# Kernel optimization log

Hardware: AMD Instinct MI355X
Metric: run time of the kernel (lower is better)

Reference implementation:

```python
import jax, jax.numpy as jnp
import numpy as np

E = 8          # num_experts
K = 2          # top_k
CAPF = 1.25    # capacity_factor


def setup_inputs() -> dict:
    key = jax.random.key(0)
    ks = jax.random.split(key, 6)
    B, T, C = 4, 2048, 1024
    x = jax.random.normal(ks[0], (B, T, C), jnp.float32)
    noise = jax.random.normal(ks[1], (B, T, E), jnp.float32)  # stands in for torch.randn_like
    Wr = jax.random.normal(ks[2], (C, E), jnp.float32) * 0.02   # topkroute_linear
    Wn = jax.random.normal(ks[3], (C, E), jnp.float32) * 0.02   # noise_linear
    W1 = jax.random.normal(ks[4], (E, C, 4 * C), jnp.float32) * 0.02  # expert up-proj
    W2 = jax.random.normal(ks[5], (E, 4 * C, C), jnp.float32) * 0.02  # expert down-proj
    return {"x": x, "noise": noise, "Wr": Wr, "Wn": Wn, "W1": W1, "W2": W2}


def reference(x, noise, Wr, Wn, W1, W2):
    B, T, C = x.shape
    N = B * T
    cap = int(N * K / E * CAPF)  # expert_capacity (static)

    # --- NoisyTopkRouter ---
    logits = x @ Wr                                  # [B,T,E]
    noise_logits = x @ Wn                            # [B,T,E]
    noisy = logits + noise * jax.nn.softplus(noise_logits)
    _, idx = jax.lax.top_k(noisy, K)                 # [B,T,K]
    mask_bte = (idx[..., None] == jnp.arange(E)).any(axis=-2)       # [B,T,E]
    gating = jax.nn.softmax(jnp.where(mask_bte, noisy, -jnp.inf), axis=-1)

    flat_x = x.reshape(N, C)
    flat_g = gating.reshape(N, E)

    # --- capacity-limited dispatch (token order, first `cap` per expert) ---
    mask = mask_bte.reshape(N, E).T                  # [E,N]
    rank = jnp.cumsum(mask, axis=1) - 1              # position within expert
    keep = mask & (rank < cap)
    slot = jnp.where(keep, rank, cap)                # overflow -> dump slot `cap`
    tok = jnp.where(keep, jnp.arange(N)[None, :], N) # dropped -> pad token `N`
    s2t = jnp.full((E, cap + 1), N, dtype=jnp.int32)
    s2t = s2t.at[jnp.arange(E)[:, None], slot].set(tok.astype(jnp.int32))[:, :cap]  # [E,cap]

    # --- gather, grouped GEMM (Linear-SiLU-Linear), weight, scatter-add ---
    x_pad = jnp.concatenate([flat_x, jnp.zeros((1, C), flat_x.dtype)], axis=0)
    xin = x_pad[s2t]                                 # [E,cap,C]
    h = jax.nn.silu(jnp.einsum('enc,ech->enh', xin, W1))
    out = jnp.einsum('enh,ehc->enc', h, W2)          # [E,cap,C]
    g_pad = jnp.concatenate([flat_g, jnp.zeros((1, E), flat_g.dtype)], axis=0)
    gate = g_pad[s2t, jnp.arange(E)[:, None]]        # [E,cap]
    weighted = out * gate[..., None]
    upd = jnp.zeros((N + 1, C), x.dtype).at[s2t.reshape(-1)].add(weighted.reshape(-1, C))
    return upd[:N].reshape(B, T, C)
```

## Files before the change

kernel.cpp:

```cpp
#include <hip/hip_runtime.h>
#include <hip/hip_bf16.h>
#include <math.h>

#define C_DIM 1024
#define H_DIM 4096
#define E_NUM 8

typedef __bf16 bf16x8 __attribute__((ext_vector_type(8)));
typedef float f32x4 __attribute__((ext_vector_type(4)));

__device__ __forceinline__ unsigned short f2bf(float f) {
  union { float f; unsigned u; } v; v.f = f;
  unsigned r = v.u + 0x7FFFu + ((v.u >> 16) & 1u);
  return (unsigned short)(r >> 16);
}

__device__ __forceinline__ void gload16(const short* g, short* l) {
  __builtin_amdgcn_global_load_lds(
      (const __attribute__((address_space(1))) unsigned int*)g,
      (__attribute__((address_space(3))) unsigned int*)l, 16, 0, 0);
}

__global__ __launch_bounds__(256) void router_kernel(
    const float* __restrict__ x, const float* __restrict__ noise,
    const float* __restrict__ Wr, const float* __restrict__ Wn,
    int2* __restrict__ idx_out, float2* __restrict__ gate_out, int N)
{
  int t = blockIdx.x;
  int tid = threadIdx.x;
  const float* xrow = x + (size_t)t * C_DIM;
  float accR[E_NUM], accN[E_NUM];
#pragma unroll
  for (int e = 0; e < E_NUM; e++) { accR[e] = 0.f; accN[e] = 0.f; }
  for (int c = tid; c < C_DIM; c += 256) {
    float xv = xrow[c];
    const float* wr = Wr + (size_t)c * E_NUM;
    const float* wn = Wn + (size_t)c * E_NUM;
#pragma unroll
    for (int e = 0; e < E_NUM; e++) {
      accR[e] = fmaf(xv, wr[e], accR[e]);
      accN[e] = fmaf(xv, wn[e], accN[e]);
    }
  }
#pragma unroll
  for (int e = 0; e < E_NUM; e++) {
    for (int off = 32; off > 0; off >>= 1) {
      accR[e] += __shfl_down(accR[e], off, 64);
      accN[e] += __shfl_down(accN[e], off, 64);
    }
  }
  __shared__ float red[4][2 * E_NUM];
  int lane = tid & 63, wave = tid >> 6;
  if (lane == 0) {
#pragma unroll
    for (int e = 0; e < E_NUM; e++) { red[wave][e] = accR[e]; red[wave][E_NUM + e] = accN[e]; }
  }
  __syncthreads();
  if (tid == 0) {
    float ns[E_NUM];
#pragma unroll
    for (int e = 0; e < E_NUM; e++) {
      float lg = red[0][e] + red[1][e] + red[2][e] + red[3][e];
      float nl = red[0][E_NUM + e] + red[1][E_NUM + e] + red[2][E_NUM + e] + red[3][E_NUM + e];
      float sp = fmaxf(nl, 0.f) + log1pf(expf(-fabsf(nl)));
      ns[e] = lg + noise[(size_t)t * E_NUM + e] * sp;
    }
    int i1 = 0; float m1 = ns[0];
    int i2 = -1; float m2 = -INFINITY;
#pragma unroll
    for (int e = 1; e < E_NUM; e++) {
      float v = ns[e];
      if (v > m1) { m2 = m1; i2 = i1; m1 = v; i1 = e; }
      else if (v > m2) { m2 = v; i2 = e; }
    }
    float e2 = expf(m2 - m1);
    float s = 1.f + e2;
    gate_out[t] = make_float2(1.f / s, e2 / s);
    idx_out[t] = make_int2(i1, i2);
  }
}

__global__ __launch_bounds__(256) void scan_kernel(
    const int2* __restrict__ idx, const float2* __restrict__ gates,
    int* __restrict__ s2t, float* __restrict__ gslot, int* __restrict__ counts,
    int N, int cap)
{
  int e = blockIdx.x;
  int tid = threadIdx.x;
  for (int s = tid; s < cap; s += 256) { s2t[(size_t)e * cap + s] = N; gslot[(size_t)e * cap + s] = 0.f; }
  __syncthreads();
  __shared__ int wtot[4];
  int lane = tid & 63, wave = tid >> 6;
  int running = 0;
  for (int base = 0; base < N; base += 256) {
    int t = base + tid;
    int2 ix = idx[t];
    bool flag = (ix.x == e) || (ix.y == e);
    unsigned long long m = __ballot(flag);
    int rank = __popcll(m & ((1ull << lane) - 1ull));
    if (lane == 0) wtot[wave] = __popcll(m);
    __syncthreads();
    int woff = 0;
    for (int w = 0; w < wave; w++) woff += wtot[w];
    int slot = running + woff + rank;
    if (flag && slot < cap) {
      s2t[(size_t)e * cap + slot] = t;
      gslot[(size_t)e * cap + slot] = (ix.x == e) ? gates[t].x : gates[t].y;
    }
    running += wtot[0] + wtot[1] + wtot[2] + wtot[3];
    __syncthreads();
  }
  if (tid == 0) counts[e] = min(running, cap);
}

__global__ __launch_bounds__(256) void convert_x_kernel(
    const float* __restrict__ src, short* __restrict__ dst, int n8)
{
  int i = blockIdx.x * 256 + threadIdx.x;
  if (i >= n8) return;
  const float4* s = (const float4*)src + (size_t)i * 2;
  float4 a = s[0], b = s[1];
  union { unsigned short us[8]; uint4 v; } o;
  o.us[0] = f2bf(a.x); o.us[1] = f2bf(a.y); o.us[2] = f2bf(a.z); o.us[3] = f2bf(a.w);
  o.us[4] = f2bf(b.x); o.us[5] = f2bf(b.y); o.us[6] = f2bf(b.z); o.us[7] = f2bf(b.w);
  ((uint4*)dst)[i] = o.v;
}

__global__ __launch_bounds__(256) void transpose_convert_kernel(
    const float* __restrict__ src, short* __restrict__ dst,
    int R, int Cc)
{
  src += (size_t)blockIdx.z * R * Cc;
  dst += (size_t)blockIdx.z * (size_t)R * Cc;
  __shared__ float tile[64][65];
  int c0 = blockIdx.x * 64, r0 = blockIdx.y * 64;
  int tid = threadIdx.x;
  int tr = tid >> 4, tc = (tid & 15) * 4;
#pragma unroll
  for (int p = 0; p < 4; p++) {
    int r = p * 16 + tr;
    float4 v = *(const float4*)(src + (size_t)(r0 + r) * Cc + c0 + tc);
    tile[r][tc] = v.x; tile[r][tc + 1] = v.y; tile[r][tc + 2] = v.z; tile[r][tc + 3] = v.w;
  }
  __syncthreads();
#pragma unroll
  for (int p = 0; p < 4; p++) {
    int c = p * 16 + tr;
    union { unsigned short us[4]; ushort4 v; } o;
#pragma unroll
    for (int j = 0; j < 4; j++) o.us[j] = f2bf(tile[tc + j][c]);
    *(ushort4*)(dst + (size_t)(c0 + c) * R + r0 + tc) = o.v;
  }
}

template<int MODE>
__global__ __launch_bounds__(512, 2) void gemm_moe(
    const short* __restrict__ Abase, const short* __restrict__ Wt,
    const int* __restrict__ s2t, const float* __restrict__ gslot,
    const int* __restrict__ counts, void* __restrict__ outp,
    int cap, int N, int rows)
{
  __shared__ short As[2][8192];
  __shared__ short Bs[2][8192];

  int flat = blockIdx.x;
  int e = flat & 7;
  int s = flat >> 3;
  int r = s % rows;
  int t = s / rows;
  int c, kc;
  if (MODE == 0) { c = t; kc = 0; }
  else           { c = t & 3; kc = t >> 2; }

  int cnt = counts[e];
  int row0 = r * 256;
  if (row0 >= cnt) return;
  int col0 = c * 256;

  int tid = threadIdx.x;
  int w = tid >> 6, l = tid & 63;
  int wr = w >> 2, wc = w & 3;
  int rowT = tid & 255, kbT = tid >> 8;

  const int NS = 32;

  const short *pA, *pB;
  if (MODE == 0) {
    int tok = min(s2t[(size_t)e * cap + row0 + rowT], N - 1);
    pA = Abase + (size_t)tok * C_DIM;
    pB = Wt + (size_t)e * (C_DIM * H_DIM) + (size_t)(col0 + rowT) * C_DIM;
  } else {
    pA = Abase + ((size_t)e * cap + row0 + rowT) * H_DIM + kc * 1024;
    pB = Wt + (size_t)e * (C_DIM * H_DIM) + (size_t)(col0 + rowT) * H_DIM + kc * 1024;
  }

  int aBase = (l >> 4) * 2048 + (wr * 128 + (l & 15)) * 8;
  int bBase = (l >> 4) * 2048 + (wc * 64 + (l & 15)) * 8;

  f32x4 acc[8][4];
#pragma unroll
  for (int m = 0; m < 8; m++)
#pragma unroll
    for (int n = 0; n < 4; n++) acc[m][n] = 0.f;

#define STAGE(k0, buf) { \
  gload16(pA + (k0) + kbT * 8,       &As[buf][kbT * 2048 + rowT * 8]); \
  gload16(pA + (k0) + (kbT + 2) * 8, &As[buf][(kbT + 2) * 2048 + rowT * 8]); \
  gload16(pB + (k0) + kbT * 8,       &Bs[buf][kbT * 2048 + rowT * 8]); \
  gload16(pB + (k0) + (kbT + 2) * 8, &Bs[buf][(kbT + 2) * 2048 + rowT * 8]); }

  STAGE(0, 0);
  int cur = 0;
#pragma unroll 1
  for (int i = 0; i < NS; ++i) {
    __syncthreads();
    bf16x8 af[8], bg[4];
#pragma unroll
    for (int m = 0; m < 8; m++)
      af[m] = *(const bf16x8*)&As[cur][aBase + m * 128];
#pragma unroll
    for (int n = 0; n < 4; n++)
      bg[n] = *(const bf16x8*)&Bs[cur][bBase + n * 128];
    if (i + 1 < NS) STAGE((i + 1) * 32, cur ^ 1);
#pragma unroll
    for (int m = 0; m < 8; m++)
#pragma unroll
      for (int n = 0; n < 4; n++)
        acc[m][n] = __builtin_amdgcn_mfma_f32_16x16x32_bf16(af[m], bg[n], acc[m][n], 0, 0, 0);
    cur ^= 1;
  }
#undef STAGE

  int orow = row0 + wr * 128 + (l >> 4) * 4;
  int ocol = col0 + wc * 64 + (l & 15);
  if (MODE == 0) {
    short* hE = (short*)outp + (size_t)e * cap * H_DIM;
#pragma unroll
    for (int m = 0; m < 8; m++)
#pragma unroll
      for (int rr = 0; rr < 4; rr++) {
        int slot = orow + m * 16 + rr;
        float g = gslot[(size_t)e * cap + slot];
        size_t rb = (size_t)slot * H_DIM + ocol;
#pragma unroll
        for (int n = 0; n < 4; n++) {
          float v = acc[m][n][rr];
          hE[rb + n * 16] = (short)f2bf(g * (v / (1.f + expf(-v))));
        }
      }
  } else {
    float* out = (float*)outp;
#pragma unroll
    for (int m = 0; m < 8; m++)
#pragma unroll
      for (int rr = 0; rr < 4; rr++) {
        int slot = orow + m * 16 + rr;
        int tok = s2t[(size_t)e * cap + slot];
        if (tok < N) {
          float* op = out + (size_t)tok * C_DIM + ocol;
#pragma unroll
          for (int n = 0; n < 4; n++)
            atomicAdd(op + n * 16, acc[m][n][rr]);
        }
      }
  }
}

extern "C" void kernel_launch(void* const* d_in, const int* in_sizes, int n_in,
                              void* d_out, int out_size, void* d_ws, size_t ws_size,
                              hipStream_t stream)
{
  const float* x     = (const float*)d_in[0];
  const float* noise = (const float*)d_in[1];
  const float* Wr    = (const float*)d_in[2];
  const float* Wn    = (const float*)d_in[3];
  const float* W1    = (const float*)d_in[4];
  const float* W2    = (const float*)d_in[5];
  float* out = (float*)d_out;

  int N = in_sizes[0] / C_DIM;
  int cap = (int)((double)N * 2.0 / E_NUM * 1.25);
  int rows = cap / 256;

  size_t off = 0;
  auto alloc = [&](size_t bytes) -> char* {
    char* r = (char*)d_ws + off;
    off += (bytes + 255) & ~(size_t)255;
    return r;
  };
  int2*   idx    = (int2*)alloc((size_t)N * sizeof(int2));
  float2* gates  = (float2*)alloc((size_t)N * sizeof(float2));
  int*    s2t    = (int*)alloc((size_t)E_NUM * cap * sizeof(int));
  float*  gslot  = (float*)alloc((size_t)E_NUM * cap * sizeof(float));
  int*    counts = (int*)alloc(E_NUM * sizeof(int));
  short*  xbf    = (short*)alloc((size_t)N * C_DIM * sizeof(short));
  short*  W1t    = (short*)alloc((size_t)E_NUM * C_DIM * H_DIM * sizeof(short));
  short*  W2t    = (short*)alloc((size_t)E_NUM * C_DIM * H_DIM * sizeof(short));
  short*  h      = (short*)alloc((size_t)E_NUM * cap * H_DIM * sizeof(short));
  (void)ws_size;

  hipMemsetAsync(d_out, 0, (size_t)out_size * sizeof(float), stream);
  router_kernel<<<N, 256, 0, stream>>>(x, noise, Wr, Wn, idx, gates, N);
  scan_kernel<<<E_NUM, 256, 0, stream>>>(idx, gates, s2t, gslot, counts, N, cap);
  convert_x_kernel<<<(N * C_DIM / 8 + 255) / 256, 256, 0, stream>>>(x, xbf, N * C_DIM / 8);
  transpose_convert_kernel<<<dim3(H_DIM / 64, C_DIM / 64, E_NUM), 256, 0, stream>>>(
      W1, W1t, C_DIM, H_DIM);
  transpose_convert_kernel<<<dim3(C_DIM / 64, H_DIM / 64, E_NUM), 256, 0, stream>>>(
      W2, W2t, H_DIM, C_DIM);

  gemm_moe<0><<<dim3(E_NUM * rows * (H_DIM / 256)), 512, 0, stream>>>(
      xbf, W1t, s2t, gslot, counts, h, cap, N, rows);
  gemm_moe<1><<<dim3(E_NUM * rows * 4 * 4), 512, 0, stream>>>(
      h, W2t, s2t, gslot, counts, out, cap, N, rows);
}
```

Baseline: 860.1 us.

## Triple-buffer LDS in MoE GEMM with explicit vmcnt waits and inline ds_reads

Moves the grouped GEMM mainloop from double to triple buffering, so two K-stages of global-to-LDS loads are in flight. The full __syncthreads is replaced by a precise vmcnt wait plus s_barrier, LDS fragments are read with inline-asm ds_read_b128 using immediate offsets, and s_setprio is raised around the MFMA block. The goal is to hide global load latency behind the matrix math. In exchange, LDS use grows from 64KB to 96KB per block, which may stop two blocks from fitting per CU as the launch bounds request. The hand-written waitcnt logic also carries correctness risk.

```diff
diff --git a/kernel.cpp b/kernel.cpp
--- a/kernel.cpp
+++ b/kernel.cpp
@@ -8,6 +8,7 @@
 
 typedef __bf16 bf16x8 __attribute__((ext_vector_type(8)));
 typedef float f32x4 __attribute__((ext_vector_type(4)));
+typedef unsigned u32x4 __attribute__((ext_vector_type(4)));
 
 __device__ __forceinline__ unsigned short f2bf(float f) {
   union { float f; unsigned u; } v; v.f = f;
@@ -20,6 +21,16 @@
       (const __attribute__((address_space(1))) unsigned int*)g,
       (__attribute__((address_space(3))) unsigned int*)l, 16, 0, 0);
 }
+
+__device__ __forceinline__ f32x4 mfma16(u32x4 a, u32x4 b, f32x4 c) {
+  return __builtin_amdgcn_mfma_f32_16x16x32_bf16(
+      __builtin_bit_cast(bf16x8, a), __builtin_bit_cast(bf16x8, b), c, 0, 0, 0);
+}
+
+#define DSR(v, a, imm) asm volatile("ds_read_b128 %0, %1 offset:" #imm : "=v"(v) : "v"(a))
+#define LGKM0 { asm volatile("s_waitcnt lgkmcnt(0)" ::: "memory"); __builtin_amdgcn_sched_barrier(0); }
+#define VMW(n) asm volatile("s_waitcnt vmcnt(" #n ")" ::: "memory")
+#define LDS_U32(p) ((unsigned)(size_t)(__attribute__((address_space(3))) short*)(p))
 
 __global__ __launch_bounds__(256) void router_kernel(
     const float* __restrict__ x, const float* __restrict__ noise,
@@ -160,8 +171,8 @@
     const int* __restrict__ counts, void* __restrict__ outp,
     int cap, int N, int rows)
 {
-  __shared__ short As[2][8192];
-  __shared__ short Bs[2][8192];
+  __shared__ short As[3][8192];
+  __shared__ short Bs[3][8192];
 
   int flat = blockIdx.x;
   int e = flat & 7;
@@ -194,8 +205,8 @@
     pB = Wt + (size_t)e * (C_DIM * H_DIM) + (size_t)(col0 + rowT) * H_DIM + kc * 1024;
   }
 
-  int aBase = (l >> 4) * 2048 + (wr * 128 + (l & 15)) * 8;
-  int bBase = (l >> 4) * 2048 + (wc * 64 + (l & 15)) * 8;
+  unsigned aB = LDS_U32(As) + (unsigned)((l >> 4) * 4096 + (wr * 128 + (l & 15)) * 16);
+  unsigned bB = LDS_U32(Bs) + (unsigned)((l >> 4) * 4096 + (wc * 64 + (l & 15)) * 16);
 
   f32x4 acc[8][4];
 #pragma unroll
@@ -210,24 +221,37 @@
   gload16(pB + (k0) + (kbT + 2) * 8, &Bs[buf][(kbT + 2) * 2048 + rowT * 8]); }
 
   STAGE(0, 0);
-  int cur = 0;
+  STAGE(32, 1);
+
+  unsigned bufR = 0;
+  int bufS = 2;
 #pragma unroll 1
   for (int i = 0; i < NS; ++i) {
-    __syncthreads();
-    bf16x8 af[8], bg[4];
+    if (i == NS - 1) { VMW(0); } else { VMW(4); }
+    __builtin_amdgcn_s_barrier();
+    __builtin_amdgcn_sched_barrier(0);
+
+    u32x4 af[8], bg[4];
+    unsigned aA = aB + bufR, bA = bB + bufR;
+    DSR(af[0], aA, 0);    DSR(af[1], aA, 256);  DSR(af[2], aA, 512);  DSR(af[3], aA, 768);
+    DSR(af[4], aA, 1024); DSR(af[5], aA, 1280); DSR(af[6], aA, 1536); DSR(af[7], aA, 1792);
+    DSR(bg[0], bA, 0);    DSR(bg[1], bA, 256);  DSR(bg[2], bA, 512);  DSR(bg[3], bA, 768);
+
+    if (i + 2 < NS) {
+      STAGE((i + 2) * 32, bufS);
+      bufS = (bufS == 2) ? 0 : bufS + 1;
+    }
+
+    LGKM0;
+    __builtin_amdgcn_s_setprio(1);
 #pragma unroll
     for (int m = 0; m < 8; m++)
-      af[m] = *(const bf16x8*)&As[cur][aBase + m * 128];
-#pragma unroll
-    for (int n = 0; n < 4; n++)
-      bg[n] = *(const bf16x8*)&Bs[cur][bBase + n * 128];
-    if (i + 1 < NS) STAGE((i + 1) * 32, cur ^ 1);
-#pragma unroll
-    for (int m = 0; m < 8; m++)
 #pragma unroll
       for (int n = 0; n < 4; n++)
-        acc[m][n] = __builtin_amdgcn_mfma_f32_16x16x32_bf16(af[m], bg[n], acc[m][n], 0, 0, 0);
-    cur ^= 1;
+        acc[m][n] = mfma16(af[m], bg[n], acc[m][n]);
+    __builtin_amdgcn_s_setprio(0);
+
+    bufR = (bufR == 32768u) ? 0u : bufR + 16384u;
   }
 #undef STAGE
 
```

New measurement: 810.4 us. 5.8% less time.
